# Kernel tuning notes

Measured on AMD Instinct MI355X. Metric: run time of the kernel, lower is better.

Reference implementation:

```python
import jax, jax.numpy as jnp
import numpy as np

FOCAL_DEFAULT = 1000.0
UNDISTORT_ITERS = 5  # cv2.undistortPoints default iteration count


def _undistort_points(pts, K, dist):
    # pts: [P,2] pixel coords; K: [3,3]; dist: [5] = (k1,k2,p1,p2,k3)
    fx, fy, cx, cy = K[0, 0], K[1, 1], K[0, 2], K[1, 2]
    x0 = (pts[:, 0] - cx) / fx
    y0 = (pts[:, 1] - cy) / fy
    k1, k2, p1, p2, k3 = dist[0], dist[1], dist[2], dist[3], dist[4]
    x, y = x0, y0
    for _ in range(UNDISTORT_ITERS):
        r2 = x * x + y * y
        icdist = 1.0 / (1.0 + ((k3 * r2 + k2) * r2 + k1) * r2)
        dx = 2.0 * p1 * x * y + p2 * (r2 + 2.0 * x * x)
        dy = p1 * (r2 + 2.0 * y * y) + 2.0 * p2 * x * y
        x = (x0 - dx) * icdist
        y = (y0 - dy) * icdist
    # re-project with cam_mat_2 == cam_mat_1 (as in the torch code)
    return jnp.stack([fx * x + cx, fy * y + cy], axis=-1)


def _compute_box_3d(dim, location, rotation_y):
    # dim: [B,P,3] = (h, w, l); location: [B,P,3]; rotation_y: [B,P]
    h, w, l = dim[..., 0], dim[..., 1], dim[..., 2]
    z0 = jnp.zeros_like(h)
    xc = jnp.stack([l / 2, l / 2, -l / 2, -l / 2, l / 2, l / 2, -l / 2, -l / 2], -1)
    yc = jnp.stack([z0, z0, z0, z0, -h, -h, -h, -h], -1)
    zc = jnp.stack([w / 2, -w / 2, -w / 2, w / 2, w / 2, -w / 2, -w / 2, w / 2], -1)
    c = jnp.cos(rotation_y)[..., None]
    s = jnp.sin(rotation_y)[..., None]
    x = c * xc + s * zc
    z = -s * xc + c * zc
    return jnp.stack([x, yc, z], -1) + location[:, :, None, :]  # [B,P,8,3]


def setup_inputs():
    key = jax.random.key(0)
    ks = jax.random.split(key, 12)
    B, P, W, H = 8, 512, 32, 32
    pre_cls_map = jax.random.normal(ks[0], (B, P, 1, W, H), jnp.float32)
    pre_2d_offset = jax.random.normal(ks[1], (B, P, 2, W, H), jnp.float32)
    pre_3d_offset = jax.random.normal(ks[2], (B, P, 2, W, H), jnp.float32)
    pre_depth = jax.random.normal(ks[3], (B, P, 1, W, H), jnp.float32)
    pre_dim = jax.random.uniform(ks[4], (B, P, 3), jnp.float32, 0.5, 4.0)
    pre_rot = jax.random.normal(ks[5], (B, P, 2), jnp.float32)
    batch_dim = jax.random.uniform(ks[6], (B, P, 3), jnp.float32, 0.5, 4.0)
    batch_rot_y = jax.random.uniform(ks[7], (B, P, 1), jnp.float32, -np.pi, np.pi)
    xz = jax.random.uniform(ks[8], (B, P, 2), jnp.float32, -20.0, 20.0)
    zz = jax.random.uniform(ks[9], (B, P, 1), jnp.float32, 5.0, 60.0)
    batch_loc = jnp.concatenate([xz, zz], -1)
    x0y0 = jax.random.uniform(ks[10], (B, P, 2), jnp.float32, 0.0, 600.0)
    wh = jax.random.uniform(ks[11], (B, P, 2), jnp.float32, 20.0, 220.0)
    rois = jnp.concatenate([x0y0, x0y0 + wh], -1)  # valid xyxy boxes
    calib = jnp.tile(jnp.array([[1000.0, 0.0, 960.0, 0.1],
                                [0.0, 1000.0, 540.0, 0.05],
                                [0.0, 0.0, 1.0, 0.2]], jnp.float32)[None], (B, 1, 1))
    trans_mat = jnp.tile(jnp.array([[0.5, 0.0, 10.0],
                                    [0.0, 0.5, 5.0]], jnp.float32)[None], (B, 1, 1))
    dist_coeffs = jnp.zeros((B, 5), jnp.float32)
    return {"batch_loc": batch_loc, "batch_dim": batch_dim, "batch_rot_y": batch_rot_y,
            "rois": rois, "pre_cls_map": pre_cls_map, "pre_2d_offset": pre_2d_offset,
            "pre_3d_offset": pre_3d_offset, "pre_depth": pre_depth, "pre_dim": pre_dim,
            "pre_rot": pre_rot, "calib": calib, "trans_mat": trans_mat,
            "dist_coeffs": dist_coeffs}


def reference(batch_loc, batch_dim, batch_rot_y, rois, pre_cls_map, pre_2d_offset,
              pre_3d_offset, pre_depth, pre_dim, pre_rot, calib, trans_mat, dist_coeffs):
    B, P, _, W, H = pre_cls_map.shape
    F = W * H
    cls = pre_cls_map.reshape(B, P, F)
    o2x = pre_2d_offset[:, :, 0].reshape(B, P, F)
    o2y = pre_2d_offset[:, :, 1].reshape(B, P, F)
    o3x = pre_3d_offset[:, :, 0].reshape(B, P, F)
    o3y = pre_3d_offset[:, :, 1].reshape(B, P, F)
    dep = pre_depth.reshape(B, P, F)
    idx = jnp.argmax(cls, axis=-1)  # [B,P]
    gather = lambda a: jnp.take_along_axis(a, idx[..., None], axis=-1)[..., 0]
    ix = (idx % W).astype(jnp.float32)
    iy = jnp.floor(idx.astype(jnp.float32) / W)
    g2x, g2y = gather(o2x), gather(o2y)
    g3x, g3y = gather(o3x), gather(o3y)
    gdep = gather(dep)
    scales_x = W / (rois[:, :, 2] - rois[:, :, 0] + 1.0)
    scales_y = H / (rois[:, :, 3] - rois[:, :, 1] + 1.0)
    pred_2d_x = (ix + g2x) / scales_x + rois[:, :, 0]
    pred_2d_y = (iy + g2y) / scales_y + rois[:, :, 1]
    center_2d = jnp.stack([pred_2d_x, pred_2d_y], -1)  # [B,P,2]
    pad = jnp.broadcast_to(jnp.array([[[0.0, 0.0, 1.0]]], jnp.float32), (B, 1, 3))
    T = jnp.concatenate([trans_mat, pad], axis=1)
    Tinv = jnp.linalg.inv(T)
    ones = jnp.ones((B, P, 1), center_2d.dtype)
    aff = jnp.einsum('bij,bpj->bpi', Tinv, jnp.concatenate([center_2d, ones], -1))[..., :2]
    und = jax.vmap(_undistort_points)(aff, calib[:, :3, :3], dist_coeffs)  # [B,P,2]
    fscale = (calib[:, 0, 0] / FOCAL_DEFAULT)[:, None]  # [B,1]
    depth = (1.0 / (jax.nn.sigmoid(gdep) + 1e-6) - 1.0) * fscale
    # unproject 2d->3d with 3x4 projection matrix
    z = depth - calib[:, 2, 3][:, None]
    x3 = (und[..., 0] * depth - calib[:, 0, 3][:, None] - calib[:, 0, 2][:, None] * z) / calib[:, 0, 0][:, None]
    y3 = (und[..., 1] * depth - calib[:, 1, 3][:, None] - calib[:, 1, 2][:, None] * z) / calib[:, 1, 1][:, None]
    x3 = x3 + g3x * fscale
    y3 = y3 + g3y * fscale
    locations = jnp.stack([x3, y3 + pre_dim[:, :, 1] / 2.0, z], -1)
    rot_sin, rot_cos = pre_rot[:, :, 0], pre_rot[:, :, 1]
    alpha = jnp.arctan(rot_sin / (rot_cos + 1e-7))
    alpha = alpha + jnp.where(rot_cos < 0, 1.0, -1.0) * (np.pi / 2.0)
    theta = jnp.arctan(locations[..., 0] / (locations[..., 2] + 1e-7))
    ry = alpha + theta
    ry = ry + (jnp.where(ry < -np.pi, 1.0, 0.0) - jnp.where(ry > np.pi, 1.0, 0.0)) * 2.0 * np.pi
    pred_c3d = _compute_box_3d(pre_dim, locations, ry)
    gt_c3d = _compute_box_3d(batch_dim, batch_loc, batch_rot_y[..., 0])
    pred_bev = pred_c3d[:, :, :4][..., (0, 2)]  # [B,P,4,2]
    gt_bev = gt_c3d[:, :, :4][..., (0, 2)]
    pmin = jnp.min(pred_bev, axis=-2); pmax = jnp.max(pred_bev, axis=-2)
    gmin = jnp.min(gt_bev, axis=-2); gmax = jnp.max(gt_bev, axis=-2)
    s1 = (pmax[..., 0] - pmin[..., 0]) * (pmax[..., 1] - pmin[..., 1])
    s2 = (gmax[..., 0] - gmin[..., 0]) * (gmax[..., 1] - gmin[..., 1])
    w = jnp.maximum(jnp.minimum(pmax[..., 0], gmax[..., 0]) - jnp.maximum(pmin[..., 0], gmin[..., 0]), 0.0)
    h = jnp.maximum(jnp.minimum(pmax[..., 1], gmax[..., 1]) - jnp.maximum(pmin[..., 1], gmin[..., 1]), 0.0)
    overlap = w * h
    iou = overlap / (s1 + s2 - overlap + 1e-6)
    return iou[..., None]  # [B,P,1], matching torch's [..., [0]] indexing
```

## Files before the change

kernel.cpp:

```cpp
#include <hip/hip_runtime.h>
#include <math.h>

#define PI_F    3.14159265358979323846f
#define PIO2_F  1.57079632679489661923f

__device__ __forceinline__ float fast_atan(float x) {
    float a = __builtin_fabsf(x);
    bool inv = a > 1.0f;
    float t = inv ? __fdividef(1.0f, a) : a;
    float t2 = t * t;
    float p = -0.0040540580f;
    p = fmaf(p, t2,  0.0218612288f);
    p = fmaf(p, t2, -0.0559098861f);
    p = fmaf(p, t2,  0.0964200441f);
    p = fmaf(p, t2, -0.1390853351f);
    p = fmaf(p, t2,  0.1994653599f);
    p = fmaf(p, t2, -0.3332985605f);
    p = fmaf(p, t2,  0.9999993329f);
    float r = t * p;
    if (inv) r = PIO2_F - r;
    return copysignf(r, x);
}

__global__ __launch_bounds__(256) void rcnn_sparse3d_loss_kernel(
    const float* __restrict__ batch_loc,
    const float* __restrict__ batch_dim,
    const float* __restrict__ batch_rot_y,
    const float* __restrict__ rois,
    const float* __restrict__ cls,
    const float* __restrict__ off2,
    const float* __restrict__ off3,
    const float* __restrict__ dep,
    const float* __restrict__ pre_dim,
    const float* __restrict__ pre_rot,
    const float* __restrict__ calib,
    const float* __restrict__ trans,
    const float* __restrict__ distc,
    float* __restrict__ out,
    int N, int Pn, int wmask, int wshift)
{
    const int wave = threadIdx.x >> 6;
    const int lane = threadIdx.x & 63;
    const int bp   = blockIdx.x * 4 + wave;
    if (bp >= N) return;
    const int b = bp / Pn;

    const float* r  = rois      + (size_t)bp * 4;
    const float r0 = r[0], r1 = r[1], r2 = r[2], r3 = r[3];
    const float* t  = trans     + (size_t)b * 6;
    const float ta = t[0], tb = t[1], tc = t[2], td = t[3], te = t[4], tf = t[5];
    const float* K  = calib     + (size_t)b * 12;
    const float fx = K[0], cx = K[2], Tx = K[3];
    const float fy = K[5], cy = K[6], Ty = K[7], Tz = K[11];
    const float* dc = distc     + (size_t)b * 5;
    const float k1 = dc[0], k2 = dc[1], p1 = dc[2], p2 = dc[3], k3 = dc[4];
    const float* pr = pre_rot   + (size_t)bp * 2;
    const float rs = pr[0], rc = pr[1];
    const float* pd = pre_dim   + (size_t)bp * 3;
    const float pdw = pd[1], pdl = pd[2];
    const float* gd = batch_dim + (size_t)bp * 3;
    const float gdw = gd[1], gdl = gd[2];
    const float* gl = batch_loc + (size_t)bp * 3;
    const float glx = gl[0], glz = gl[2];
    const float gry = batch_rot_y[bp];

    const float4* c4 = reinterpret_cast<const float4*>(cls + (size_t)bp * 1024);
    float bestv = -INFINITY;
    int   besti = 0;
    #pragma unroll
    for (int j = 0; j < 4; ++j) {
        float4 v = c4[j * 64 + lane];
        int base = 4 * (j * 64 + lane);
        if (v.x > bestv) { bestv = v.x; besti = base;     }
        if (v.y > bestv) { bestv = v.y; besti = base + 1; }
        if (v.z > bestv) { bestv = v.z; besti = base + 2; }
        if (v.w > bestv) { bestv = v.w; besti = base + 3; }
    }
    #pragma unroll
    for (int s = 1; s < 64; s <<= 1) {
        float ov = __shfl_xor(bestv, s);
        int   oi = __shfl_xor(besti, s);
        if (ov > bestv || (ov == bestv && oi < besti)) { bestv = ov; besti = oi; }
    }
    const int idx = besti;

    const size_t o2b = (size_t)bp * 2048;
    const float g2x  = off2[o2b + idx];
    const float g2y  = off2[o2b + 1024 + idx];
    const float g3x  = off3[o2b + idx];
    const float g3y  = off3[o2b + 1024 + idx];
    const float gdep = dep[(size_t)bp * 1024 + idx];

    const float Wf = (float)(wmask + 1);
    const float invW = __frcp_rn(Wf);
    const float ix = (float)(idx & wmask);
    const float iy = (float)(idx >> wshift);
    const float px = (ix + g2x) * (r2 - r0 + 1.0f) * invW + r0;
    const float py = (iy + g2y) * (r3 - r1 + 1.0f) * invW + r1;

    const float invdet = __frcp_rn(ta * te - tb * td);
    const float ax = ( te * px - tb * py + (tb * tf - tc * te)) * invdet;
    const float ay = (-td * px + ta * py + (tc * td - ta * tf)) * invdet;

    const float x0 = (ax - cx) * __frcp_rn(fx);
    const float y0 = (ay - cy) * __frcp_rn(fy);
    float ux = x0, uy = y0;
    if (!(k1 == 0.0f && k2 == 0.0f && p1 == 0.0f && p2 == 0.0f && k3 == 0.0f)) {
        #pragma unroll
        for (int it = 0; it < 5; ++it) {
            const float rr2 = ux * ux + uy * uy;
            const float icd = __fdividef(1.0f, 1.0f + ((k3 * rr2 + k2) * rr2 + k1) * rr2);
            const float dx  = 2.0f * p1 * ux * uy + p2 * (rr2 + 2.0f * ux * ux);
            const float dy  = p1 * (rr2 + 2.0f * uy * uy) + 2.0f * p2 * ux * uy;
            ux = (x0 - dx) * icd;
            uy = (y0 - dy) * icd;
        }
    }
    const float undx = fx * ux + cx;
    const float undy = fy * uy + cy;

    const float fscale = fx * 0.001f;
    const float sig    = __fdividef(1.0f, 1.0f + __expf(-gdep));
    const float depth  = (__fdividef(1.0f, sig + 1e-6f) - 1.0f) * fscale;
    const float z3     = depth - Tz;
    const float invfx  = __frcp_rn(fx);
    const float invfy  = __frcp_rn(fy);
    float x3 = (undx * depth - Tx - cx * z3) * invfx;
    x3 += g3x * fscale;

    float alpha = fast_atan(__fdividef(rs, rc + 1e-7f)) + (rc < 0.0f ? PIO2_F : -PIO2_F);
    const float theta = fast_atan(__fdividef(x3, z3 + 1e-7f));
    float ry = alpha + theta;
    if (ry < -PI_F) ry += 2.0f * PI_F;
    else if (ry > PI_F) ry -= 2.0f * PI_F;

    float pcc, pss, gcc, gss;
    __sincosf(ry,  &pss, &pcc);
    __sincosf(gry, &gss, &gcc);

    auto bev_minmax = [](float w, float l, float lx, float lz, float cc, float ss,
                         float& mnx, float& mxx, float& mnz, float& mxz) {
        const float hx = l * 0.5f, hz = w * 0.5f;
        const float ex = __builtin_fabsf(cc * hx) + __builtin_fabsf(ss * hz);
        const float ez = __builtin_fabsf(ss * hx) + __builtin_fabsf(cc * hz);
        mnx = lx - ex; mxx = lx + ex;
        mnz = lz - ez; mxz = lz + ez;
    };

    float pmnx, pmxx, pmnz, pmxz, gmnx, gmxx, gmnz, gmxz;
    bev_minmax(pdw, pdl, x3,  z3,  pcc, pss, pmnx, pmxx, pmnz, pmxz);
    bev_minmax(gdw, gdl, glx, glz, gcc, gss, gmnx, gmxx, gmnz, gmxz);

    const float s1 = (pmxx - pmnx) * (pmxz - pmnz);
    const float s2 = (gmxx - gmnx) * (gmxz - gmnz);
    const float ww = fmaxf(fminf(pmxx, gmxx) - fmaxf(pmnx, gmnx), 0.0f);
    const float hh = fmaxf(fminf(pmxz, gmxz) - fmaxf(pmnz, gmnz), 0.0f);
    const float ov = ww * hh;
    const float iou = __fdividef(ov, s1 + s2 - ov + 1e-6f);

    if (lane == 0) out[bp] = iou;
}

extern "C" void kernel_launch(void* const* d_in, const int* in_sizes, int n_in,
                              void* d_out, int out_size, void* d_ws, size_t ws_size,
                              hipStream_t stream) {
    const float* batch_loc   = (const float*)d_in[0];
    const float* batch_dim   = (const float*)d_in[1];
    const float* batch_rot_y = (const float*)d_in[2];
    const float* rois        = (const float*)d_in[3];
    const float* pre_cls     = (const float*)d_in[4];
    const float* pre_2d      = (const float*)d_in[5];
    const float* pre_3d      = (const float*)d_in[6];
    const float* pre_depth   = (const float*)d_in[7];
    const float* pre_dim     = (const float*)d_in[8];
    const float* pre_rot     = (const float*)d_in[9];
    const float* calib       = (const float*)d_in[10];
    const float* trans_mat   = (const float*)d_in[11];
    const float* dist_coeffs = (const float*)d_in[12];
    float* out = (float*)d_out;

    const int N  = in_sizes[2];
    const int Bn = in_sizes[10] / 12;
    const int Pn = N / Bn;
    const int F  = in_sizes[4] / N;
    int Wk = 1; while (Wk * Wk < F) Wk <<= 1;
    int wshift = 0; while ((1 << wshift) < Wk) ++wshift;

    const int waves_per_block = 4;
    const int grid = (N + waves_per_block - 1) / waves_per_block;
    rcnn_sparse3d_loss_kernel<<<grid, 256, 0, stream>>>(
        batch_loc, batch_dim, batch_rot_y, rois, pre_cls, pre_2d, pre_3d,
        pre_depth, pre_dim, pre_rot, calib, trans_mat, dist_coeffs,
        out, N, Pn, Wk - 1, wshift);
}
```

Measured before the change: 9.627 us.

## Split each row's argmax across two waves and combine via shared memory

Each ROI row's 1024-element class-map argmax is now split between two wavefronts, each scanning half, and the partial results are combined through LDS after a block barrier. The grid doubles to two rows per block so more waves are in flight and per-wave serial load latency shrinks. In exchange it adds a __syncthreads, duplicates the scalar tail computation in both waves, and introduces a barrier after a possible early return for out-of-range rows. Unused Ty/undy/invfy values are also removed.

```diff
diff --git a/kernel.cpp b/kernel.cpp
--- a/kernel.cpp
+++ b/kernel.cpp
@@ -39,9 +39,14 @@
     float* __restrict__ out,
     int N, int Pn, int wmask, int wshift)
 {
+    __shared__ float s_val[4];
+    __shared__ int   s_idx[4];
+
     const int wave = threadIdx.x >> 6;
     const int lane = threadIdx.x & 63;
-    const int bp   = blockIdx.x * 4 + wave;
+    const int pair = wave >> 1;
+    const int half = wave & 1;
+    const int bp   = blockIdx.x * 2 + pair;
     if (bp >= N) return;
     const int b = bp / Pn;
 
@@ -51,7 +56,7 @@
     const float ta = t[0], tb = t[1], tc = t[2], td = t[3], te = t[4], tf = t[5];
     const float* K  = calib     + (size_t)b * 12;
     const float fx = K[0], cx = K[2], Tx = K[3];
-    const float fy = K[5], cy = K[6], Ty = K[7], Tz = K[11];
+    const float fy = K[5], cy = K[6], Tz = K[11];
     const float* dc = distc     + (size_t)b * 5;
     const float k1 = dc[0], k2 = dc[1], p1 = dc[2], p2 = dc[3], k3 = dc[4];
     const float* pr = pre_rot   + (size_t)bp * 2;
@@ -64,13 +69,14 @@
     const float glx = gl[0], glz = gl[2];
     const float gry = batch_rot_y[bp];
 
-    const float4* c4 = reinterpret_cast<const float4*>(cls + (size_t)bp * 1024);
+    const float4* c4 = reinterpret_cast<const float4*>(cls + (size_t)bp * 1024) + half * 128;
+    const int idx_base = half * 512;
     float bestv = -INFINITY;
     int   besti = 0;
     #pragma unroll
-    for (int j = 0; j < 4; ++j) {
+    for (int j = 0; j < 2; ++j) {
         float4 v = c4[j * 64 + lane];
-        int base = 4 * (j * 64 + lane);
+        int base = idx_base + 4 * (j * 64 + lane);
         if (v.x > bestv) { bestv = v.x; besti = base;     }
         if (v.y > bestv) { bestv = v.y; besti = base + 1; }
         if (v.z > bestv) { bestv = v.z; besti = base + 2; }
@@ -81,6 +87,14 @@
         float ov = __shfl_xor(bestv, s);
         int   oi = __shfl_xor(besti, s);
         if (ov > bestv || (ov == bestv && oi < besti)) { bestv = ov; besti = oi; }
+    }
+
+    if (lane == 0) { s_val[wave] = bestv; s_idx[wave] = besti; }
+    __syncthreads();
+    {
+        const float v0 = s_val[pair * 2],     v1 = s_val[pair * 2 + 1];
+        const int   i0 = s_idx[pair * 2],     i1 = s_idx[pair * 2 + 1];
+        if (v1 > v0 || (v1 == v0 && i1 < i0)) { besti = i1; } else { besti = i0; }
     }
     const int idx = besti;
 
@@ -117,15 +131,12 @@
         }
     }
     const float undx = fx * ux + cx;
-    const float undy = fy * uy + cy;
 
     const float fscale = fx * 0.001f;
     const float sig    = __fdividef(1.0f, 1.0f + __expf(-gdep));
     const float depth  = (__fdividef(1.0f, sig + 1e-6f) - 1.0f) * fscale;
     const float z3     = depth - Tz;
-    const float invfx  = __frcp_rn(fx);
-    const float invfy  = __frcp_rn(fy);
-    float x3 = (undx * depth - Tx - cx * z3) * invfx;
+    float x3 = (undx * depth - Tx - cx * z3) * __frcp_rn(fx);
     x3 += g3x * fscale;
 
     float alpha = fast_atan(__fdividef(rs, rc + 1e-7f)) + (rc < 0.0f ? PIO2_F : -PIO2_F);
@@ -158,7 +169,7 @@
     const float ov = ww * hh;
     const float iou = __fdividef(ov, s1 + s2 - ov + 1e-6f);
 
-    if (lane == 0) out[bp] = iou;
+    if (half == 0 && lane == 0) out[bp] = iou;
 }
 
 extern "C" void kernel_launch(void* const* d_in, const int* in_sizes, int n_in,
@@ -186,8 +197,8 @@
     int Wk = 1; while (Wk * Wk < F) Wk <<= 1;
     int wshift = 0; while ((1 << wshift) < Wk) ++wshift;
 
-    const int waves_per_block = 4;
-    const int grid = (N + waves_per_block - 1) / waves_per_block;
+    const int rows_per_block = 2;
+    const int grid = (N + rows_per_block - 1) / rows_per_block;
     rcnn_sparse3d_loss_kernel<<<grid, 256, 0, stream>>>(
         batch_loc, batch_dim, batch_rot_y, rois, pre_cls, pre_2d, pre_3d,
         pre_depth, pre_dim, pre_rot, calib, trans_mat, dist_coeffs,
```

After: 11.37 us. 18.1% more time.
